# Performance work log

Measured on AMD Instinct MI355X. Metric: run time of the kernel, lower is better.

Reference implementation:

```python
import jax, jax.numpy as jnp
import numpy as np

N, D, C, S, E, K, MIN_MATCH, N_ITER = 100000, 128, 16, 16, 3200000, 64, 1, 4


def setup_inputs() -> dict:
    key = jax.random.key(0)
    k1, k2, k3, k4 = jax.random.split(key, 4)
    es = jax.random.normal(k1, (N, D), jnp.float32)
    edge_index = jax.random.randint(k2, (2, E), 0, N)
    seeds = jax.random.randint(k3, (C, S), 0, N)
    W = jax.random.normal(k4, (D, D), jnp.float32) / np.float32(np.sqrt(D))
    return {"es": es, "edge_index": edge_index, "seeds": seeds, "W": W, "n_iter": N_ITER}


def _memory_step(es, idx, hx, W):
    # ragged gather of last expansion, padded to fixed size per class: [C, k, D]
    inp = es[idx]
    d = inp.shape[-1]
    q = jnp.mean(inp, axis=1) if hx is None else hx          # attention query [C, D]
    logits = jnp.einsum('ckd,cd->ck', inp, q) / jnp.sqrt(jnp.float32(d))
    a = jax.nn.softmax(logits, axis=-1)                      # [C, k]
    ctx = jnp.einsum('ck,ckd->cd', a, inp)                   # attended read [C, D]
    pre = ctx if hx is None else ctx + hx                    # recurrent memory update
    return jnp.tanh(pre @ W)                                 # [C, D]


def _cosine(x, y):
    xn = x / (jnp.linalg.norm(x, axis=-1, keepdims=True) + 1e-8)
    yn = y / (jnp.linalg.norm(y, axis=-1, keepdims=True) + 1e-8)
    return xn @ yn.T                                         # [N, C]


def _expand(es, W, edge_index, seeds, n_iter):
    n, c = es.shape[0], seeds.shape[0]
    src, dst = edge_index[0], edge_index[1]
    # known_mask.scatter_(0, seed_all, 1)
    known = jnp.zeros((n,), bool).at[seeds.ravel()].set(True)
    # get_cate_mask(seeds, N): per-class membership mask [C, N]
    cate = jnp.zeros((c, n), bool).at[jnp.arange(c)[:, None], seeds].set(True)
    hx, last = None, seeds
    outs, exps, hxes = [], [], []
    for _ in range(n_iter):
        hx = _memory_step(es, last, hx, W)
        # get_cate_neighbors: per-class count of in-edges whose source is in the class
        counts = jax.vmap(lambda m: jax.ops.segment_sum(m, dst, num_segments=n))(
            cate.astype(jnp.float32)[:, src])                # [C, N]
        valid = (counts >= MIN_MATCH) & (~known)[None, :]    # [C, N]
        scores = _cosine(es, hx).T                           # [C, N]
        # _select: top n_expansion valid nodes per class (finite fill avoids -inf grads)
        probs, idx = jax.lax.top_k(jnp.where(valid, scores, -1e9), K)
        known = known.at[idx.ravel()].set(True)
        cate = cate.at[jnp.arange(c)[:, None], idx].set(True)
        last = idx
        outs.append(probs); exps.append(idx); hxes.append(hx)
    return jnp.stack(outs), jnp.stack(exps), jnp.stack(hxes)


def reference(es, edge_index, seeds, W, n_iter):
    return _expand(es, W, edge_index, seeds, n_iter)
```

## Files before the change

kernel.cpp:

```cpp
#include <hip/hip_runtime.h>
#include <math.h>

#define NN 100000
#define DD 128
#define CC 16
#define SS 16
#define EE 3200000
#define KK 64
#define NIT 4
#define CNT_STRIDE 32
#define NB 32
#define SLMAX 4096
#define MM (NB * KK)
#define EB ((EE + 255) / 256)
#define INF_STAMP 0x7fffffff

typedef unsigned long long ull;

__device__ inline ull ordkey(double d) {
    long long b = __double_as_longlong(d);
    return (b < 0) ? ~(ull)b : ((ull)b | 0x8000000000000000ULL);
}
__device__ inline double keyord(ull u) {
    long long b = (u & 0x8000000000000000ULL)
                    ? (long long)(u & 0x7FFFFFFFFFFFFFFFULL)
                    : (long long)~u;
    return __longlong_as_double(b);
}
__device__ inline bool gt(ull ka, int na, ull kb, int nb) {
    return (ka > kb) || (ka == kb && na < nb);
}

__device__ inline void wsort64(ull& k, int& n, int lane) {
    for (int k2 = 2; k2 <= 64; k2 <<= 1) {
        for (int j = k2 >> 1; j; j >>= 1) {
            ull ok = __shfl_xor(k, j, 64);
            int on = __shfl_xor(n, j, 64);
            bool isLow = (lane & j) == 0;
            bool d = (k2 == 64) || ((lane & k2) == 0);
            bool wantMax = (d == isLow);
            if (wantMax == gt(ok, on, k, n)) { k = ok; n = on; }
        }
    }
}
__device__ inline void wmerge64(ull& k, int& n, int lane) {
    for (int j = 32; j; j >>= 1) {
        ull ok = __shfl_xor(k, j, 64);
        int on = __shfl_xor(n, j, 64);
        bool wantMax = (lane & j) == 0;
        if (wantMax == gt(ok, on, k, n)) { k = ok; n = on; }
    }
}


__global__ __launch_bounds__(256)
void k_init(const float* __restrict__ es, double* __restrict__ inv_norm,
            int* __restrict__ known, unsigned* __restrict__ cate,
            unsigned* __restrict__ nbr) {
    int wave = threadIdx.x >> 6, lane = threadIdx.x & 63;
    int n = blockIdx.x * 4 + wave;
    if (n >= NN) return;
    float a = es[(long)n * DD + lane];
    float b = es[(long)n * DD + 64 + lane];
    double p = (double)a * (double)a + (double)b * (double)b;
    for (int o = 32; o > 0; o >>= 1) p += __shfl_xor(p, o, 64);
    if (lane == 0) {
        inv_norm[n] = 1.0 / (sqrt(p) + 1e-8);
        known[n] = INF_STAMP;
        cate[n] = 0;
        nbr[n] = 0;
    }
}

__global__ void k_seed(const int* __restrict__ seeds, int* __restrict__ known,
                       unsigned* __restrict__ cate) {
    int i = threadIdx.x;
    if (i < CC * SS) {
        int n = seeds[i];
        known[n] = 0;
        atomicOr(&cate[n], 1u << (i / SS));
    }
}


__global__ __launch_bounds__(256)
void k_memedge(const float* __restrict__ es, const float* __restrict__ Wm,
               const int* __restrict__ seeds, const int* __restrict__ last,
               double* __restrict__ hx, double* __restrict__ hxn,
               float* __restrict__ out, int* __restrict__ cnt,
               const int* __restrict__ edge, const unsigned* __restrict__ cate,
               unsigned* __restrict__ nbr, int t) {
    __shared__ float  inp[KK][DD + 1];
    __shared__ int    rowS[KK];
    __shared__ double q[DD];
    __shared__ double lg[KK];
    __shared__ double sr[KK];
    __shared__ double pre[DD];
    __shared__ double red[DD];
    int tid = threadIdx.x;

    if (blockIdx.x >= CC) {
        long e = (long)(blockIdx.x - CC) * 256 + tid;
        if (e < EE) {
            int s = edge[e];
            unsigned m = cate[s];
            if (m) {
                int d = edge[EE + e];
                atomicOr(&nbr[d], m);
            }
        }
        return;
    }

    int c = blockIdx.x;
    if (tid == 0) cnt[c * CNT_STRIDE] = 0;
    int k = (t == 0) ? SS : KK;
    if (tid < KK) {
        lg[tid] = -1.0e308;
        if (tid < k) rowS[tid] = (t == 0) ? seeds[c * SS + tid] : last[c * KK + tid];
    }
    __syncthreads();
    for (int i = tid; i < k * DD; i += 256)
        inp[i >> 7][i & 127] = es[(long)rowS[i >> 7] * DD + (i & 127)];
    __syncthreads();
    if (tid < DD) {
        if (t == 0) {
            double s = 0;
            for (int j = 0; j < k; ++j) s += (double)inp[j][tid];
            q[tid] = s / (double)k;
        } else {
            q[tid] = hx[c * DD + tid];
        }
    }
    __syncthreads();
    if (tid < k) {
        double s = 0;
        for (int i = 0; i < DD; ++i) s += (double)inp[tid][i] * q[i];
        lg[tid] = s / sqrt((double)DD);
    }
    __syncthreads();
    if (tid < KK) sr[tid] = lg[tid];
    __syncthreads();
    for (int st = 32; st > 0; st >>= 1) {
        if (tid < st) sr[tid] = fmax(sr[tid], sr[tid + st]);
        __syncthreads();
    }
    double mx = sr[0];
    __syncthreads();
    if (tid < KK) {
        double e = (tid < k) ? exp(lg[tid] - mx) : 0.0;
        lg[tid] = e; sr[tid] = e;
    }
    __syncthreads();
    for (int st = 32; st > 0; st >>= 1) {
        if (tid < st) sr[tid] += sr[tid + st];
        __syncthreads();
    }
    double sm = sr[0];
    __syncthreads();
    if (tid < KK) lg[tid] /= sm;
    __syncthreads();
    if (tid < DD) {
        double ctx = 0;
        for (int j = 0; j < k; ++j) ctx += lg[j] * (double)inp[j][tid];
        pre[tid] = (t == 0) ? ctx : (ctx + q[tid]);
    }
    __syncthreads();
    double h = 0;
    if (tid < DD) {
        for (int i = 0; i < DD; ++i) h += pre[i] * (double)Wm[i * DD + tid];
        h = tanh(h);
        red[tid] = h * h;
    }
    __syncthreads();
    for (int st = 64; st > 0; st >>= 1) {
        if (tid < st) red[tid] += red[tid + st];
        __syncthreads();
    }
    if (tid < DD) {
        double inv = 1.0 / (sqrt(red[0]) + 1e-8);
        hx[c * DD + tid] = h;
        hxn[c * DD + tid] = h * inv;
        out[2 * NIT * CC * KK + t * CC * DD + c * DD + tid] = (float)h;
    }
}


__global__ __launch_bounds__(256)
void k_cand(const float* __restrict__ es, const double* __restrict__ inv_norm,
            const int* __restrict__ known, const unsigned* __restrict__ nbr,
            const double* __restrict__ hxn,
            int* __restrict__ cnt, int* __restrict__ cidx,
            ull* __restrict__ ckey, int cap, int t) {
    __shared__ int    pair[256 * 16];
    __shared__ short  prank[256 * 16];
    __shared__ double hxnL[CC * 129];
    __shared__ int    lcnt[CC];
    __shared__ int    base[CC];
    __shared__ int    npair;
    int tid = threadIdx.x;

    for (int i = tid; i < CC * DD; i += 256)
        hxnL[(i >> 7) * 129 + (i & 127)] = hxn[i];
    if (tid < CC) lcnt[tid] = 0;
    if (tid == 0) npair = 0;
    __syncthreads();

    int n = blockIdx.x * 256 + tid;
    unsigned m = 0;
    if (n < NN && known[n] > t) m = nbr[n];
    while (m) {
        int c = __ffs(m) - 1;
        m &= m - 1;
        int r = atomicAdd(&lcnt[c], 1);
        int p = atomicAdd(&npair, 1);
        pair[p] = (n << 4) | c;
        prank[p] = (short)r;
    }
    __syncthreads();

    if (tid < CC && lcnt[tid] > 0)
        base[tid] = atomicAdd(&cnt[tid * CNT_STRIDE], lcnt[tid]);
    __syncthreads();

    int np = npair;
    for (int t2 = tid; t2 < np; t2 += 256) {
        int pk = pair[t2];
        int nn = pk >> 4, c = pk & 15;
        const float4* row = (const float4*)(es + (long)nn * DD);
        const double* h = &hxnL[c * 129];
        double s = 0;
        #pragma unroll
        for (int i = 0; i < 32; ++i) {
            float4 v = row[i];
            s += (double)v.x * h[4 * i + 0] + (double)v.y * h[4 * i + 1]
               + (double)v.z * h[4 * i + 2] + (double)v.w * h[4 * i + 3];
        }
        int pos = base[c] + (int)prank[t2];
        if (pos < cap) {
            cidx[(long)c * cap + pos] = nn;
            ckey[(long)c * cap + pos] = ordkey(s * inv_norm[nn]);
        }
    }
}


__global__ __launch_bounds__(256)
void k_top(const int* __restrict__ cnt, const int* __restrict__ cidx,
           const ull* __restrict__ ckey, int cap,
           ull* __restrict__ tkey, int* __restrict__ tnode) {
    __shared__ ull ks[SLMAX];
    __shared__ int ns[SLMAX];
    int c = blockIdx.x / NB, b = blockIdx.x % NB;
    int tid = threadIdx.x, wave = tid >> 6, lane = tid & 63;
    int count = min(cnt[c * CNT_STRIDE], cap);
    int per = (count + NB - 1) / NB;
    int start = b * per;
    int m = min(per, count - start);
    int sl = 64;
    while (sl < per) sl <<= 1;
    int nruns = sl >> 6;
    for (int r = wave; r < nruns; r += 4) {
        int i = (r << 6) + lane;
        ull k; int n;
        if (i < m) { k = ckey[(long)c * cap + start + i]; n = cidx[(long)c * cap + start + i]; }
        else       { k = 0ULL; n = 0x7FFFFFFF; }
        wsort64(k, n, lane);
        ks[i] = k; ns[i] = n;
    }
    __syncthreads();
    for (int step = 1; step < nruns; step <<= 1) {
        int npair2 = nruns / (2 * step);
        for (int pr = wave; pr < npair2; pr += 4) {
            int ra = pr * 2 * step, rb = ra + step;
            ull ka = ks[(ra << 6) + lane];       int na = ns[(ra << 6) + lane];
            ull kb = ks[(rb << 6) + 63 - lane];  int nb2 = ns[(rb << 6) + 63 - lane];
            if (gt(kb, nb2, ka, na)) { ka = kb; na = nb2; }
            wmerge64(ka, na, lane);
            ks[(ra << 6) + lane] = ka; ns[(ra << 6) + lane] = na;
        }
        __syncthreads();
    }
    if (tid < KK) {
        tkey[(long)c * MM + b * KK + tid] = ks[tid];
        tnode[(long)c * MM + b * KK + tid] = ns[tid];
    }
}


__global__ __launch_bounds__(256)
void k_mergeupd(const int* __restrict__ cnt,
                const ull* __restrict__ tkey, const int* __restrict__ tnode,
                int* __restrict__ known, const unsigned* __restrict__ nbr,
                unsigned* __restrict__ cate, int* __restrict__ last,
                float* __restrict__ out, int cap, int t) {
    __shared__ ull ks[MM];
    __shared__ int ns[MM];
    int c = blockIdx.x, tid = threadIdx.x, wave = tid >> 6, lane = tid & 63;
    for (int i = tid; i < MM; i += 256) {
        ks[i] = tkey[(long)c * MM + i];
        ns[i] = tnode[(long)c * MM + i];
    }
    __syncthreads();
    for (int step = 1; step < NB; step <<= 1) {
        int npair2 = NB / (2 * step);
        for (int pr = wave; pr < npair2; pr += 4) {
            int ra = pr * 2 * step, rb = ra + step;
            ull ka = ks[(ra << 6) + lane];       int na = ns[(ra << 6) + lane];
            ull kb = ks[(rb << 6) + 63 - lane];  int nb2 = ns[(rb << 6) + 63 - lane];
            if (gt(kb, nb2, ka, na)) { ka = kb; na = nb2; }
            wmerge64(ka, na, lane);
            ks[(ra << 6) + lane] = ka; ns[(ra << 6) + lane] = na;
        }
        __syncthreads();
    }
    int count = min(cnt[c * CNT_STRIDE], cap);
    int nsel = min(count, KK);
    if (tid < KK && tid < nsel) {
        int n = ns[tid];
        out[t * CC * KK + c * KK + tid] = (float)keyord(ks[tid]);
        out[NIT * CC * KK + t * CC * KK + c * KK + tid] = (float)n;
        last[c * KK + tid] = n;
        known[n] = t + 1;
        atomicOr(&cate[n], 1u << c);
    }
    if (tid == 0 && nsel < KK) {
        int r = nsel;
        for (int n = 0; n < NN && r < KK; ++n) {
            bool valid = ((nbr[n] >> c) & 1u) && (known[n] > t);
            if (!valid) {
                out[t * CC * KK + c * KK + r] = -1e9f;
                out[NIT * CC * KK + t * CC * KK + c * KK + r] = (float)n;
                last[c * KK + r] = n;
                known[n] = t + 1;
                atomicOr(&cate[n], 1u << c);
                ++r;
            }
        }
    }
}


extern "C" void kernel_launch(void* const* d_in, const int* in_sizes, int n_in,
                              void* d_out, int out_size, void* d_ws, size_t ws_size,
                              hipStream_t stream) {
    const float* es    = (const float*)d_in[0];
    const int*   edge  = (const int*)d_in[1];
    const int*   seeds = (const int*)d_in[2];
    const float* W     = (const float*)d_in[3];
    float* out = (float*)d_out;

    char* p = (char*)d_ws;
    auto alloc = [&](size_t bytes) -> char* {
        char* r = p;
        p += (bytes + 255) & ~(size_t)255;
        return r;
    };
    double*   inv_norm = (double*)alloc((size_t)NN * 8);
    int*      known    = (int*)alloc((size_t)NN * 4);
    unsigned* cate     = (unsigned*)alloc((size_t)NN * 4);
    unsigned* nbr      = (unsigned*)alloc((size_t)NN * 4);
    double*   hx       = (double*)alloc(CC * DD * 8);
    double*   hxn      = (double*)alloc(CC * DD * 8);
    int*      last     = (int*)alloc(CC * KK * 4);
    int*      cnt      = (int*)alloc(CC * CNT_STRIDE * 4);
    ull*      tkey     = (ull*)alloc((size_t)CC * MM * 8);
    int*      tnode    = (int*)alloc((size_t)CC * MM * 4);
    size_t used = (size_t)(p - (char*)d_ws);
    size_t rem = (ws_size > used + 8192) ? (ws_size - used - 8192) : 0;
    long capl = (long)(rem / (CC * 12));
    if (capl > NN) capl = NN;
    if (capl < 1) capl = 1;
    int cap = (int)capl;
    int*    cidx = (int*)alloc((size_t)CC * cap * 4);
    ull*    ckey = (ull*)alloc((size_t)CC * cap * 8);

    k_init<<<(NN + 3) / 4, 256, 0, stream>>>(es, inv_norm, known, cate, nbr);
    k_seed<<<1, 256, 0, stream>>>(seeds, known, cate);

    for (int t = 0; t < NIT; ++t) {
        k_memedge<<<CC + EB, 256, 0, stream>>>(es, W, seeds, last, hx, hxn, out,
                                               cnt, edge, cate, nbr, t);
        k_cand<<<(NN + 255) / 256, 256, 0, stream>>>(es, inv_norm, known, nbr, hxn,
                                                     cnt, cidx, ckey, cap, t);
        k_top<<<CC * NB, 256, 0, stream>>>(cnt, cidx, ckey, cap, tkey, tnode);
        k_mergeupd<<<CC, 256, 0, stream>>>(cnt, tkey, tnode, known, nbr,
                                           cate, last, out, cap, t);
    }
}
```

Before: 310.3 us.

## Fuse seed init, drop norm precompute, grid-stride edges, single-kernel top-k

Folds seed marking into the init kernel and stops reading all of es to precompute inverse norms; candidate norms are now computed on the fly in k_cand from the row it already loads. The edge scan becomes a grid-stride loop over a fixed 2048 blocks instead of one block per 256 edges. The two-stage top-k (32 blocks per class plus a merge kernel) is replaced by one block per class that streams candidates through a running top-64 per wave. This cuts kernel launches and a full pass over es, but the per-class top-k now runs on only 16 blocks and can become serial if candidate counts are large.

```diff
diff --git a/kernel.cpp b/kernel.cpp
--- a/kernel.cpp
+++ b/kernel.cpp
@@ -9,10 +9,7 @@
 #define KK 64
 #define NIT 4
 #define CNT_STRIDE 32
-#define NB 32
-#define SLMAX 4096
-#define MM (NB * KK)
-#define EB ((EE + 255) / 256)
+#define EBLK 2048
 #define INF_STAMP 0x7fffffff
 
 typedef unsigned long long ull;
@@ -54,31 +51,24 @@
 
 
 __global__ __launch_bounds__(256)
-void k_init(const float* __restrict__ es, double* __restrict__ inv_norm,
-            int* __restrict__ known, unsigned* __restrict__ cate,
-            unsigned* __restrict__ nbr) {
-    int wave = threadIdx.x >> 6, lane = threadIdx.x & 63;
+void k_init(const int* __restrict__ seeds, int* __restrict__ known,
+            unsigned* __restrict__ cate, unsigned* __restrict__ nbr) {
+    __shared__ int sd[CC * SS];
+    int tid = threadIdx.x;
+    if (tid < CC * SS) sd[tid] = seeds[tid];
+    __syncthreads();
+    int wave = tid >> 6, lane = tid & 63;
     int n = blockIdx.x * 4 + wave;
     if (n >= NN) return;
-    float a = es[(long)n * DD + lane];
-    float b = es[(long)n * DD + 64 + lane];
-    double p = (double)a * (double)a + (double)b * (double)b;
-    for (int o = 32; o > 0; o >>= 1) p += __shfl_xor(p, o, 64);
+    unsigned m = 0;
+    #pragma unroll
+    for (int e = lane; e < CC * SS; e += 64)
+        if (sd[e] == n) m |= 1u << (e / SS);
+    for (int o = 32; o > 0; o >>= 1) m |= __shfl_xor(m, o, 64);
     if (lane == 0) {
-        inv_norm[n] = 1.0 / (sqrt(p) + 1e-8);
-        known[n] = INF_STAMP;
-        cate[n] = 0;
+        known[n] = m ? 0 : INF_STAMP;
+        cate[n] = m;
         nbr[n] = 0;
-    }
-}
-
-__global__ void k_seed(const int* __restrict__ seeds, int* __restrict__ known,
-                       unsigned* __restrict__ cate) {
-    int i = threadIdx.x;
-    if (i < CC * SS) {
-        int n = seeds[i];
-        known[n] = 0;
-        atomicOr(&cate[n], 1u << (i / SS));
     }
 }
 
@@ -100,14 +90,11 @@
     int tid = threadIdx.x;
 
     if (blockIdx.x >= CC) {
-        long e = (long)(blockIdx.x - CC) * 256 + tid;
-        if (e < EE) {
+        for (long e = (long)(blockIdx.x - CC) * 256 + tid; e < EE;
+             e += (long)EBLK * 256) {
             int s = edge[e];
             unsigned m = cate[s];
-            if (m) {
-                int d = edge[EE + e];
-                atomicOr(&nbr[d], m);
-            }
+            if (m) atomicOr(&nbr[edge[EE + e]], m);
         }
         return;
     }
@@ -187,7 +174,7 @@
 
 
 __global__ __launch_bounds__(256)
-void k_cand(const float* __restrict__ es, const double* __restrict__ inv_norm,
+void k_cand(const float* __restrict__ es,
             const int* __restrict__ known, const unsigned* __restrict__ nbr,
             const double* __restrict__ hxn,
             int* __restrict__ cnt, int* __restrict__ cidx,
@@ -229,96 +216,69 @@
         int nn = pk >> 4, c = pk & 15;
         const float4* row = (const float4*)(es + (long)nn * DD);
         const double* h = &hxnL[c * 129];
-        double s = 0;
+        double s = 0, p2 = 0;
         #pragma unroll
         for (int i = 0; i < 32; ++i) {
             float4 v = row[i];
-            s += (double)v.x * h[4 * i + 0] + (double)v.y * h[4 * i + 1]
-               + (double)v.z * h[4 * i + 2] + (double)v.w * h[4 * i + 3];
+            double vx = v.x, vy = v.y, vz = v.z, vw = v.w;
+            s  += vx * h[4 * i + 0] + vy * h[4 * i + 1]
+                + vz * h[4 * i + 2] + vw * h[4 * i + 3];
+            p2 += vx * vx + vy * vy + vz * vz + vw * vw;
         }
         int pos = base[c] + (int)prank[t2];
         if (pos < cap) {
             cidx[(long)c * cap + pos] = nn;
-            ckey[(long)c * cap + pos] = ordkey(s * inv_norm[nn]);
+            ckey[(long)c * cap + pos] = ordkey(s / (sqrt(p2) + 1e-8));
         }
     }
 }
 
 
 __global__ __launch_bounds__(256)
-void k_top(const int* __restrict__ cnt, const int* __restrict__ cidx,
-           const ull* __restrict__ ckey, int cap,
-           ull* __restrict__ tkey, int* __restrict__ tnode) {
-    __shared__ ull ks[SLMAX];
-    __shared__ int ns[SLMAX];
-    int c = blockIdx.x / NB, b = blockIdx.x % NB;
-    int tid = threadIdx.x, wave = tid >> 6, lane = tid & 63;
+void k_topupd(const int* __restrict__ cnt, const int* __restrict__ cidx,
+              const ull* __restrict__ ckey,
+              int* __restrict__ known, const unsigned* __restrict__ nbr,
+              unsigned* __restrict__ cate, int* __restrict__ last,
+              float* __restrict__ out, int cap, int t) {
+    __shared__ ull ksh[4 * KK];
+    __shared__ int nsh[4 * KK];
+    int c = blockIdx.x, tid = threadIdx.x, wave = tid >> 6, lane = tid & 63;
     int count = min(cnt[c * CNT_STRIDE], cap);
-    int per = (count + NB - 1) / NB;
-    int start = b * per;
-    int m = min(per, count - start);
-    int sl = 64;
-    while (sl < per) sl <<= 1;
-    int nruns = sl >> 6;
-    for (int r = wave; r < nruns; r += 4) {
-        int i = (r << 6) + lane;
+
+    ull rk = 0ULL; int rn = 0x7FFFFFFF;
+    int nch = (count + 63) >> 6;
+    for (int ch = wave; ch < nch; ch += 4) {
+        int i = (ch << 6) + lane;
         ull k; int n;
-        if (i < m) { k = ckey[(long)c * cap + start + i]; n = cidx[(long)c * cap + start + i]; }
-        else       { k = 0ULL; n = 0x7FFFFFFF; }
+        if (i < count) { k = ckey[(long)c * cap + i]; n = cidx[(long)c * cap + i]; }
+        else           { k = 0ULL; n = 0x7FFFFFFF; }
         wsort64(k, n, lane);
-        ks[i] = k; ns[i] = n;
-    }
-    __syncthreads();
-    for (int step = 1; step < nruns; step <<= 1) {
-        int npair2 = nruns / (2 * step);
-        for (int pr = wave; pr < npair2; pr += 4) {
-            int ra = pr * 2 * step, rb = ra + step;
-            ull ka = ks[(ra << 6) + lane];       int na = ns[(ra << 6) + lane];
-            ull kb = ks[(rb << 6) + 63 - lane];  int nb2 = ns[(rb << 6) + 63 - lane];
+        ull ok = __shfl(k, 63 - lane, 64);
+        int on = __shfl(n, 63 - lane, 64);
+        if (gt(ok, on, rk, rn)) { rk = ok; rn = on; }
+        wmerge64(rk, rn, lane);
+    }
+    ksh[(wave << 6) + lane] = rk;
+    nsh[(wave << 6) + lane] = rn;
+    __syncthreads();
+
+    for (int step = 1; step < 4; step <<= 1) {
+        int npair2 = 4 / (2 * step);
+        if (wave < npair2) {
+            int ra = wave * 2 * step, rb = ra + step;
+            ull ka = ksh[(ra << 6) + lane];       int na = nsh[(ra << 6) + lane];
+            ull kb = ksh[(rb << 6) + 63 - lane];  int nb2 = nsh[(rb << 6) + 63 - lane];
             if (gt(kb, nb2, ka, na)) { ka = kb; na = nb2; }
             wmerge64(ka, na, lane);
-            ks[(ra << 6) + lane] = ka; ns[(ra << 6) + lane] = na;
+            ksh[(ra << 6) + lane] = ka; nsh[(ra << 6) + lane] = na;
         }
         __syncthreads();
     }
-    if (tid < KK) {
-        tkey[(long)c * MM + b * KK + tid] = ks[tid];
-        tnode[(long)c * MM + b * KK + tid] = ns[tid];
-    }
-}
-
-
-__global__ __launch_bounds__(256)
-void k_mergeupd(const int* __restrict__ cnt,
-                const ull* __restrict__ tkey, const int* __restrict__ tnode,
-                int* __restrict__ known, const unsigned* __restrict__ nbr,
-                unsigned* __restrict__ cate, int* __restrict__ last,
-                float* __restrict__ out, int cap, int t) {
-    __shared__ ull ks[MM];
-    __shared__ int ns[MM];
-    int c = blockIdx.x, tid = threadIdx.x, wave = tid >> 6, lane = tid & 63;
-    for (int i = tid; i < MM; i += 256) {
-        ks[i] = tkey[(long)c * MM + i];
-        ns[i] = tnode[(long)c * MM + i];
-    }
-    __syncthreads();
-    for (int step = 1; step < NB; step <<= 1) {
-        int npair2 = NB / (2 * step);
-        for (int pr = wave; pr < npair2; pr += 4) {
-            int ra = pr * 2 * step, rb = ra + step;
-            ull ka = ks[(ra << 6) + lane];       int na = ns[(ra << 6) + lane];
-            ull kb = ks[(rb << 6) + 63 - lane];  int nb2 = ns[(rb << 6) + 63 - lane];
-            if (gt(kb, nb2, ka, na)) { ka = kb; na = nb2; }
-            wmerge64(ka, na, lane);
-            ks[(ra << 6) + lane] = ka; ns[(ra << 6) + lane] = na;
-        }
-        __syncthreads();
-    }
-    int count = min(cnt[c * CNT_STRIDE], cap);
+
     int nsel = min(count, KK);
     if (tid < KK && tid < nsel) {
-        int n = ns[tid];
-        out[t * CC * KK + c * KK + tid] = (float)keyord(ks[tid]);
+        int n = nsh[tid];
+        out[t * CC * KK + c * KK + tid] = (float)keyord(ksh[tid]);
         out[NIT * CC * KK + t * CC * KK + c * KK + tid] = (float)n;
         last[c * KK + tid] = n;
         known[n] = t + 1;
@@ -356,7 +316,6 @@
         p += (bytes + 255) & ~(size_t)255;
         return r;
     };
-    double*   inv_norm = (double*)alloc((size_t)NN * 8);
     int*      known    = (int*)alloc((size_t)NN * 4);
     unsigned* cate     = (unsigned*)alloc((size_t)NN * 4);
     unsigned* nbr      = (unsigned*)alloc((size_t)NN * 4);
@@ -364,8 +323,6 @@
     double*   hxn      = (double*)alloc(CC * DD * 8);
     int*      last     = (int*)alloc(CC * KK * 4);
     int*      cnt      = (int*)alloc(CC * CNT_STRIDE * 4);
-    ull*      tkey     = (ull*)alloc((size_t)CC * MM * 8);
-    int*      tnode    = (int*)alloc((size_t)CC * MM * 4);
     size_t used = (size_t)(p - (char*)d_ws);
     size_t rem = (ws_size > used + 8192) ? (ws_size - used - 8192) : 0;
     long capl = (long)(rem / (CC * 12));
@@ -375,16 +332,14 @@
     int*    cidx = (int*)alloc((size_t)CC * cap * 4);
     ull*    ckey = (ull*)alloc((size_t)CC * cap * 8);
 
-    k_init<<<(NN + 3) / 4, 256, 0, stream>>>(es, inv_norm, known, cate, nbr);
-    k_seed<<<1, 256, 0, stream>>>(seeds, known, cate);
+    k_init<<<(NN + 3) / 4, 256, 0, stream>>>(seeds, known, cate, nbr);
 
     for (int t = 0; t < NIT; ++t) {
-        k_memedge<<<CC + EB, 256, 0, stream>>>(es, W, seeds, last, hx, hxn, out,
-                                               cnt, edge, cate, nbr, t);
-        k_cand<<<(NN + 255) / 256, 256, 0, stream>>>(es, inv_norm, known, nbr, hxn,
+        k_memedge<<<CC + EBLK, 256, 0, stream>>>(es, W, seeds, last, hx, hxn, out,
+                                                 cnt, edge, cate, nbr, t);
+        k_cand<<<(NN + 255) / 256, 256, 0, stream>>>(es, known, nbr, hxn,
                                                      cnt, cidx, ckey, cap, t);
-        k_top<<<CC * NB, 256, 0, stream>>>(cnt, cidx, ckey, cap, tkey, tnode);
-        k_mergeupd<<<CC, 256, 0, stream>>>(cnt, tkey, tnode, known, nbr,
-                                           cate, last, out, cap, t);
-    }
-}
+        k_topupd<<<CC, 256, 0, stream>>>(cnt, cidx, ckey, known, nbr,
+                                         cate, last, out, cap, t);
+    }
+}
```

Measured after the change: 375.6 us. 21.0% more time.
